# Kernel tuning notes

Hardware: AMD Instinct MI355X
Metric: run time of the kernel (lower is better)

The kernel has to match this reference:

```python
import jax, jax.numpy as jnp
import numpy as np

B, S, D, H = 4, 2048, 1024, 16
HS = D // H  # head size = 64


def setup_inputs() -> dict:
    key = jax.random.key(0)
    k1, k2, k3 = jax.random.split(key, 3)
    return {
        "input_data": jax.random.normal(k1, (B, S, D), dtype=jnp.float32),
        "w_qkv": jax.random.normal(k2, (D, 3 * D), dtype=jnp.float32) * (1.0 / np.sqrt(D)),
        "b_qkv": jnp.zeros((3 * D,), dtype=jnp.float32),
        "w_proj": jax.random.normal(k3, (D, D), dtype=jnp.float32) * (1.0 / np.sqrt(D)),
        "b_proj": jnp.zeros((D,), dtype=jnp.float32),
    }


def reference(input_data, w_qkv, b_qkv, w_proj, b_proj):
    b, s, d = input_data.shape
    qkv = input_data @ w_qkv + b_qkv  # [b, s, 3d]
    q, k, v = jnp.split(qkv, 3, axis=-1)
    # [b, h, s, hs]
    q = q.reshape(b, s, H, HS).transpose(0, 2, 1, 3)
    k = k.reshape(b, s, H, HS).transpose(0, 2, 1, 3)
    v = v.reshape(b, s, H, HS).transpose(0, 2, 1, 3)
    # NB: original module scales by 1/sqrt(num_heads), not 1/sqrt(head_size)
    scores = jnp.einsum('bhqd,bhkd->bhqk', q, k) / jnp.sqrt(jnp.float32(H))
    causal = jnp.tril(jnp.ones((s, s), dtype=bool))
    scores = jnp.where(causal[None, None], scores, -jnp.inf)
    weights = jax.nn.softmax(scores, axis=-1)  # dropout p=0.0 -> identity
    out = jnp.einsum('bhqk,bhkd->bhqd', weights, v)
    out = out.transpose(0, 2, 1, 3).reshape(b, s, d)
    return out @ w_proj + b_proj
```

## Files before the change

kernel.cpp:

```cpp
#include <hip/hip_runtime.h>


typedef unsigned short u16;
typedef short bf16x8 __attribute__((ext_vector_type(8)));
typedef unsigned short u16x8 __attribute__((ext_vector_type(8)));
typedef float f32x4 __attribute__((ext_vector_type(4)));
typedef float f32x16 __attribute__((ext_vector_type(16)));

#define S_LEN 2048
#define DMODEL 1024
#define NHEAD 16
#define MROWS 8192

#define SCALE_LOG2E 0.36067376022224085f

#define WAITVM_(N) asm volatile("s_waitcnt vmcnt(" #N ")" ::: "memory")
#define WAITVM(N) WAITVM_(N)

__device__ __forceinline__ u16 f2bf(float f) {
  union { float f; unsigned u; } c; c.f = f;
  unsigned u = c.u;
  u += 0x7fffu + ((u >> 16) & 1u);
  return (u16)(u >> 16);
}

__device__ __forceinline__ float exp2_fast(float x) {
  float r; asm("v_exp_f32 %0, %1" : "=v"(r) : "v"(x)); return r;
}

__device__ __forceinline__ unsigned cvtpk_bf16(float a, float b) {
  unsigned r;
  asm("v_cvt_pk_bf16_f32 %0, %1, %2" : "=v"(r) : "v"(a), "v"(b));
  return r;
}

__device__ __forceinline__ void plswap(unsigned& a, unsigned& b) {
  asm("v_permlane32_swap_b32 %0, %1" : "+v"(a), "+v"(b));
}

__device__ __forceinline__ f32x4 mfma16(bf16x8 a, bf16x8 b, f32x4 c) {
  return __builtin_amdgcn_mfma_f32_16x16x32_bf16(a, b, c, 0, 0, 0);
}

__device__ __forceinline__ f32x16 mfma32(bf16x8 a, bf16x8 b, f32x16 c) {
  return __builtin_amdgcn_mfma_f32_32x32x16_bf16(a, b, c, 0, 0, 0);
}

__device__ __forceinline__ void gload_lds16(const void* g, void* l) {
  __builtin_amdgcn_global_load_lds((__attribute__((address_space(1))) void*)g,
                                   (__attribute__((address_space(3))) void*)l,
                                   16, 0, 0);
}

__global__ void k_f32_to_bf16(const float* __restrict__ in, u16* __restrict__ out, int n) {
  int i = (blockIdx.x * 256 + threadIdx.x) * 4;
  if (i < n) {
    float4 v = *reinterpret_cast<const float4*>(in + i);
    ushort4 o;
    o.x = f2bf(v.x); o.y = f2bf(v.y); o.z = f2bf(v.z); o.w = f2bf(v.w);
    *reinterpret_cast<ushort4*>(out + i) = o;
  }
}

__global__ void k_transpose_to_bf16(const float* __restrict__ in, u16* __restrict__ out,
                                    int K, int N) {
  __shared__ float t[32][33];
  int n0 = blockIdx.x * 32, k0 = blockIdx.y * 32;
  int tx = threadIdx.x & 31, ty = threadIdx.x >> 5;
#pragma unroll
  for (int i = 0; i < 32; i += 8)
    t[ty + i][tx] = in[(size_t)(k0 + ty + i) * N + n0 + tx];
  __syncthreads();
#pragma unroll
  for (int i = 0; i < 32; i += 8)
    out[(size_t)(n0 + ty + i) * K + k0 + tx] = f2bf(t[tx][ty + i]);
}

template <int MODE, int BM>
__global__ __launch_bounds__(BM * 2) void k_gemm9(const u16* __restrict__ A,
                                                  const u16* __restrict__ Bt,
                                                  const float* __restrict__ bias,
                                                  u16* __restrict__ outb,
                                                  float* __restrict__ outf,
                                                  u16* __restrict__ vtout,
                                                  int N, int K) {
  constexpr int LOADS = (BM == 256) ? 3 : 4;
  __shared__ u16 As[3][BM * 32];
  __shared__ u16 Bs[3][128 * 32];

  const int tid = threadIdx.x;
  const int lane = tid & 63, wave = tid >> 6;
  const int wr = wave >> 1, wc = wave & 1;
  const int lr = lane & 15, lk = lane >> 4;
  const int m0 = blockIdx.x * BM, n0 = blockIdx.y * 128;
  const size_t Kb = (size_t)K * 2;

  const int csw = ((tid & 3) ^ ((tid >> 3) & 3)) * 16;
  const char* Asrc0 = (const char*)A + (size_t)(m0 + (tid >> 2)) * Kb + csw;
  const char* Asrc1 = Asrc0 + (size_t)(BM / 2) * Kb;
  const char* Bsrc0 = (const char*)Bt + (size_t)(n0 + (tid >> 2)) * Kb + csw;
  const char* Bsrc1 = Bsrc0 + (size_t)64 * Kb;

#define STAGE_T(BUFX, T)                                                       \
  {                                                                            \
    const size_t ko_ = (size_t)(T) * 64;                                       \
    gload_lds16(Asrc0 + ko_, &As[BUFX][(size_t)tid * 8]);                      \
    gload_lds16(Asrc1 + ko_, &As[BUFX][(size_t)tid * 8 + (size_t)BM * 16]);    \
    gload_lds16(Bsrc0 + ko_, &Bs[BUFX][(size_t)tid * 8]);                      \
    if (BM == 128)                                                             \
      gload_lds16(Bsrc1 + ko_, &Bs[BUFX][(size_t)tid * 8 + 2048]);             \
  }

  f32x4 zero4 = {0.f, 0.f, 0.f, 0.f};
  f32x4 acc[4][4];
#pragma unroll
  for (int m = 0; m < 4; ++m)
#pragma unroll
    for (int n = 0; n < 4; ++n) acc[m][n] = zero4;

  const int slotsw = (lr >> 1) & 3;

#define PHASE_T(BUFX, DOSTAGE, SBUF, ST, VMZERO)                               \
  {                                                                            \
    if (VMZERO) { WAITVM(0); }                                                 \
    else if (LOADS == 3) { WAITVM(3); }                                        \
    else { WAITVM(4); }                                                        \
    __builtin_amdgcn_s_barrier();                                              \
    __builtin_amdgcn_sched_barrier(0);                                         \
    bf16x8 af[4], bfr[4];                                                      \
    _Pragma("unroll") for (int m = 0; m < 4; ++m)                              \
        af[m] = *reinterpret_cast<const bf16x8*>(                              \
            &As[BUFX][(wr * 64 + m * 16 + lr) * 32 + ((lk ^ slotsw) * 8)]);    \
    _Pragma("unroll") for (int n = 0; n < 4; ++n)                              \
        bfr[n] = *reinterpret_cast<const bf16x8*>(                             \
            &Bs[BUFX][(wc * 64 + n * 16 + lr) * 32 + ((lk ^ slotsw) * 8)]);    \
    if (DOSTAGE) STAGE_T(SBUF, ST);                                            \
    __builtin_amdgcn_sched_barrier(0);                                         \
    __builtin_amdgcn_s_setprio(1);                                             \
    _Pragma("unroll") for (int m = 0; m < 4; ++m)                              \
        _Pragma("unroll") for (int n = 0; n < 4; ++n)                          \
            acc[m][n] = mfma16(af[m], bfr[n], acc[m][n]);                      \
    __builtin_amdgcn_s_setprio(0);                                             \
  }

  const int nkt = K >> 5;
  STAGE_T(0, 0);
  STAGE_T(1, 1);

  for (int t = 0; t < nkt - 2; ++t) {
    PHASE_T(t % 3, 1, (t + 2) % 3, t + 2, 0);
  }
  PHASE_T((nkt - 2) % 3, 0, 0, 0, 0);
  PHASE_T((nkt - 1) % 3, 0, 0, 0, 1);
#undef PHASE_T
#undef STAGE_T

#pragma unroll
  for (int n = 0; n < 4; ++n) {
    int col = n0 + wc * 64 + n * 16 + lr;
    float bv = bias[col];
#pragma unroll
    for (int m = 0; m < 4; ++m) {
      int rowb = m0 + wr * 64 + m * 16 + lk * 4;
      if (MODE == 1) {
#pragma unroll
        for (int r = 0; r < 4; ++r)
          outf[(size_t)(rowb + r) * N + col] = acc[m][n][r] + bv;
      } else {
        if (col < 2048) {
          const float qs = (col < 1024) ? SCALE_LOG2E : 1.0f;
#pragma unroll
          for (int r = 0; r < 4; ++r)
            outb[(size_t)(rowb + r) * 2048 + col] = f2bf((acc[m][n][r] + bv) * qs);
        } else {
          int hh = (col >> 6) & 15, dd = col & 63;
          int bb = rowb >> 11, ss = rowb & 2047;
          ushort4 o;
          o.x = f2bf(acc[m][n][0] + bv);
          o.y = f2bf(acc[m][n][1] + bv);
          o.z = f2bf(acc[m][n][2] + bv);
          o.w = f2bf(acc[m][n][3] + bv);
          *reinterpret_cast<ushort4*>(
              vtout + ((size_t)(bb * 16 + hh) * 64 + dd) * 2048 + ss) = o;
        }
      }
    }
  }
}

__global__ __launch_bounds__(256, 2) void k_attn14(const u16* __restrict__ qk,
                                                   const u16* __restrict__ vt,
                                                   u16* __restrict__ ao) {
  __shared__ u16 Ks[2][4096];
  __shared__ u16 Vs[2][4096];

  const int tid = threadIdx.x;
  const int lane = tid & 63, wave = tid >> 6;
  const int l31 = lane & 31, hi = lane >> 5;
  const int gid = blockIdx.x;
  const int bh = gid & 63;
  const int tq = gid >> 6;
  const int j = (tq < 4) ? tq : 11 - tq;
  const int b = bh >> 4, h = bh & 15;

  const int qbase = j * 256 + wave * 64;
  const int ktd = 4 * j + wave;
  const int KTMAX = 4 * j + 3;

  bf16x8 qf[2][4];
#pragma unroll
  for (int g = 0; g < 2; ++g) {
    const u16* qp = qk + ((size_t)b * S_LEN + qbase + g * 32 + l31) * 2048 + h * 64 + hi * 8;
#pragma unroll
    for (int ks = 0; ks < 4; ++ks)
      qf[g][ks] = *reinterpret_cast<const bf16x8*>(qp + ks * 16);
  }

  const int swzcol = 16 * ((lane & 7) ^ (lane >> 3));
  const char* kg = (const char*)qk + ((size_t)b * S_LEN) * 4096 + 2048 + h * 128 +
                   (size_t)(wave * 16 + (lane >> 3)) * 4096 + swzcol;
  const char* vg = (const char*)vt +
                   ((size_t)bh * 64 + wave * 16 + (lane >> 3)) * 4096 + swzcol;

#define STAGE(BUF, KT)                                                        \
  {                                                                           \
    const char* kg_ = kg + (size_t)(KT) * 64 * 4096;                          \
    const char* vg_ = vg + (size_t)(KT) * 128;                                \
    gload_lds16(kg_, &Ks[BUF][wave * 1024]);                                  \
    gload_lds16(kg_ + (size_t)8 * 4096, &Ks[BUF][wave * 1024 + 512]);         \
    gload_lds16(vg_, &Vs[BUF][wave * 1024]);                                  \
    gload_lds16(vg_ + (size_t)8 * 4096, &Vs[BUF][wave * 1024 + 512]);         \
  }

  f32x16 oT[2][2];
#pragma unroll
  for (int g = 0; g < 2; ++g)
#pragma unroll
    for (int kb = 0; kb < 2; ++kb)
#pragma unroll
      for (int e = 0; e < 16; ++e) oT[g][kb][e] = 0.f;
  float l_i[2] = {0.f, 0.f};

  const int rsw = (l31 & 7) << 4;

  STAGE(0, 0);
  __syncthreads();
  int buf = 0;

  for (int kt = 0; kt <= KTMAX; ++kt) {
    if (kt < KTMAX) STAGE(buf ^ 1, kt + 1);

    if (kt <= ktd) {
      const char* Kb = (const char*)&Ks[buf][0];
      const char* Vb = (const char*)&Vs[buf][0];
      const bool masked = (kt == ktd);

      bf16x8 kf[2][4];
#pragma unroll
      for (int kb = 0; kb < 2; ++kb)
#pragma unroll
        for (int ks = 0; ks < 4; ++ks)
          kf[kb][ks] = *reinterpret_cast<const bf16x8*>(
              Kb + (kb * 32 + l31) * 128 + ((ks * 32 + hi * 16) ^ rsw));

      bf16x8 vf[2][4];
#pragma unroll
      for (int kbd = 0; kbd < 2; ++kbd)
#pragma unroll
        for (int tt = 0; tt < 4; ++tt)
          vf[kbd][tt] = *reinterpret_cast<const bf16x8*>(
              Vb + (kbd * 32 + l31) * 128 + ((tt * 32 + hi * 16) ^ rsw));

#pragma unroll
      for (int g = 0; g < 2; ++g) {
        f32x16 sc[2];
        __builtin_amdgcn_s_setprio(1);
#pragma unroll
        for (int kb = 0; kb < 2; ++kb) {
          sc[kb] = mfma32(kf[kb][0], qf[g][0], f32x16{});
#pragma unroll
          for (int ks = 1; ks < 4; ++ks)
            sc[kb] = mfma32(kf[kb][ks], qf[g][ks], sc[kb]);
        }
        __builtin_amdgcn_s_setprio(0);

        if (masked) {
          const int qrel = g * 32 + l31;
#pragma unroll
          for (int kb = 0; kb < 2; ++kb)
#pragma unroll
            for (int e = 0; e < 16; ++e) {
              int key_ = kb * 32 + (e & 3) + ((e >> 2) << 3) + hi * 4;
              if (key_ > qrel) sc[kb][e] = -INFINITY;
            }
        }

        float rsa = 0.f, rsb = 0.f, rsc = 0.f, rsd = 0.f;
        unsigned pk_[8][2];
#pragma unroll
        for (int kb = 0; kb < 2; ++kb)
#pragma unroll
          for (int s = 0; s < 4; ++s) {
            float p0 = exp2_fast(sc[kb][s * 4 + 0]);
            float p1 = exp2_fast(sc[kb][s * 4 + 1]);
            float p2 = exp2_fast(sc[kb][s * 4 + 2]);
            float p3 = exp2_fast(sc[kb][s * 4 + 3]);
            rsa += p0; rsb += p1; rsc += p2; rsd += p3;
            pk_[kb * 4 + s][0] = cvtpk_bf16(p0, p1);
            pk_[kb * 4 + s][1] = cvtpk_bf16(p2, p3);
          }
        l_i[g] += (rsa + rsb) + (rsc + rsd);

        bf16x8 pfr[4];
#pragma unroll
        for (int tt = 0; tt < 4; ++tt) {
          unsigned a0 = pk_[2 * tt][0], b0 = pk_[2 * tt + 1][0];
          unsigned a1 = pk_[2 * tt][1], b1 = pk_[2 * tt + 1][1];
          plswap(a0, b0);
          plswap(a1, b1);
          unsigned fr[4] = {a0, a1, b0, b1};
          pfr[tt] = *reinterpret_cast<const bf16x8*>(&fr[0]);
        }

        __builtin_amdgcn_s_setprio(1);
#pragma unroll
        for (int tt = 0; tt < 4; ++tt) {
          oT[g][0] = mfma32(vf[0][tt], pfr[tt], oT[g][0]);
          oT[g][1] = mfma32(vf[1][tt], pfr[tt], oT[g][1]);
        }
        __builtin_amdgcn_s_setprio(0);
      }
    }

    __syncthreads();
    buf ^= 1;
  }
#undef STAGE

#pragma unroll
  for (int g = 0; g < 2; ++g) {
    float lt = l_i[g] + __shfl_xor(l_i[g], 32, 64);
    float inv = 1.f / lt;
    u16* orow = ao + ((size_t)b * S_LEN + qbase + g * 32 + l31) * DMODEL + h * 64 + hi * 4;
#pragma unroll
    for (int kbd = 0; kbd < 2; ++kbd)
#pragma unroll
      for (int s = 0; s < 4; ++s) {
        unsigned w0 = cvtpk_bf16(oT[g][kbd][s * 4 + 0] * inv, oT[g][kbd][s * 4 + 1] * inv);
        unsigned w1 = cvtpk_bf16(oT[g][kbd][s * 4 + 2] * inv, oT[g][kbd][s * 4 + 3] * inv);
        *reinterpret_cast<unsigned*>(orow + kbd * 32 + s * 8) = w0;
        *reinterpret_cast<unsigned*>(orow + kbd * 32 + s * 8 + 2) = w1;
      }
  }
}

extern "C" void kernel_launch(void* const* d_in, const int* in_sizes, int n_in,
                              void* d_out, int out_size, void* d_ws, size_t ws_size,
                              hipStream_t stream) {
  const float* x = (const float*)d_in[0];
  const float* wqkv = (const float*)d_in[1];
  const float* bqkv = (const float*)d_in[2];
  const float* wproj = (const float*)d_in[3];
  const float* bproj = (const float*)d_in[4];
  float* out = (float*)d_out;

  char* ws = (char*)d_ws;
  u16* Xb     = (u16*)(ws);
  u16* Wqkvt  = (u16*)(ws + (size_t)16777216);
  u16* Wprojt = (u16*)(ws + (size_t)23068672);
  u16* QKb    = (u16*)(ws + (size_t)25165824);
  u16* Vt     = (u16*)(ws + (size_t)58720256);
  u16* AOb    = (u16*)(ws + (size_t)75497472);

  k_f32_to_bf16<<<MROWS * DMODEL / 4 / 256, 256, 0, stream>>>(x, Xb, MROWS * DMODEL);
  k_transpose_to_bf16<<<dim3(3072 / 32, 1024 / 32), 256, 0, stream>>>(wqkv, Wqkvt, 1024, 3072);
  k_transpose_to_bf16<<<dim3(1024 / 32, 1024 / 32), 256, 0, stream>>>(wproj, Wprojt, 1024, 1024);

  k_gemm9<2, 256><<<dim3(MROWS / 256, 3072 / 128), 512, 0, stream>>>(
      Xb, Wqkvt, bqkv, QKb, nullptr, Vt, 3072, 1024);

  k_attn14<<<dim3(512), 256, 0, stream>>>(QKb, Vt, AOb);

  k_gemm9<1, 128><<<dim3(MROWS / 128, DMODEL / 128), 256, 0, stream>>>(
      AOb, Wprojt, bproj, nullptr, out, nullptr, DMODEL, 1024);
}
```

Measured before the change: 171.6 us.

## Double-buffer GEMM fragments in registers and deepen the LDS prefetch pipeline

Restructures the bf16 GEMM main loop so the LDS fragments for the next k-tile are read into a second register set while the MFMAs for the current tile run. Global-to-LDS staging now keeps three tiles in flight instead of two. N and K become compile-time constants so the loop fully unrolls with fixed waitcnt values. The aim is to hide LDS read latency behind the MFMA work and cut barrier stalls, at the cost of more vector registers for the extra fragment set and a waitcnt that is conservative for the 128-row variant.

```diff
diff --git a/kernel.cpp b/kernel.cpp
--- a/kernel.cpp
+++ b/kernel.cpp
@@ -16,6 +16,7 @@
 
 #define WAITVM_(N) asm volatile("s_waitcnt vmcnt(" #N ")" ::: "memory")
 #define WAITVM(N) WAITVM_(N)
+#define WAITLGKM0 asm volatile("s_waitcnt lgkmcnt(0)" ::: "memory")
 
 __device__ __forceinline__ u16 f2bf(float f) {
   union { float f; unsigned u; } c; c.f = f;
@@ -77,14 +78,14 @@
 }
 
 template <int MODE, int BM>
-__global__ __launch_bounds__(BM * 2) void k_gemm9(const u16* __restrict__ A,
-                                                  const u16* __restrict__ Bt,
-                                                  const float* __restrict__ bias,
-                                                  u16* __restrict__ outb,
-                                                  float* __restrict__ outf,
-                                                  u16* __restrict__ vtout,
-                                                  int N, int K) {
-  constexpr int LOADS = (BM == 256) ? 3 : 4;
+__global__ __launch_bounds__(BM * 2) void k_gemm10(const u16* __restrict__ A,
+                                                   const u16* __restrict__ Bt,
+                                                   const float* __restrict__ bias,
+                                                   u16* __restrict__ outb,
+                                                   float* __restrict__ outf,
+                                                   u16* __restrict__ vtout) {
+  const int N = (MODE == 2) ? 3072 : DMODEL;
+  const int K = 1024;
   __shared__ u16 As[3][BM * 32];
   __shared__ u16 Bs[3][128 * 32];
 
@@ -120,39 +121,59 @@
 
   const int slotsw = (lr >> 1) & 3;
 
-#define PHASE_T(BUFX, DOSTAGE, SBUF, ST, VMZERO)                               \
+#define READF(AF, BF, BUFX)                                                    \
   {                                                                            \
-    if (VMZERO) { WAITVM(0); }                                                 \
-    else if (LOADS == 3) { WAITVM(3); }                                        \
-    else { WAITVM(4); }                                                        \
-    __builtin_amdgcn_s_barrier();                                              \
-    __builtin_amdgcn_sched_barrier(0);                                         \
-    bf16x8 af[4], bfr[4];                                                      \
     _Pragma("unroll") for (int m = 0; m < 4; ++m)                              \
-        af[m] = *reinterpret_cast<const bf16x8*>(                              \
+        AF[m] = *reinterpret_cast<const bf16x8*>(                              \
             &As[BUFX][(wr * 64 + m * 16 + lr) * 32 + ((lk ^ slotsw) * 8)]);    \
     _Pragma("unroll") for (int n = 0; n < 4; ++n)                              \
-        bfr[n] = *reinterpret_cast<const bf16x8*>(                             \
+        BF[n] = *reinterpret_cast<const bf16x8*>(                              \
             &Bs[BUFX][(wc * 64 + n * 16 + lr) * 32 + ((lk ^ slotsw) * 8)]);    \
-    if (DOSTAGE) STAGE_T(SBUF, ST);                                            \
-    __builtin_amdgcn_sched_barrier(0);                                         \
+  }
+
+#define DOMFMA(AF, BF)                                                         \
+  {                                                                            \
     __builtin_amdgcn_s_setprio(1);                                             \
     _Pragma("unroll") for (int m = 0; m < 4; ++m)                              \
         _Pragma("unroll") for (int n = 0; n < 4; ++n)                          \
-            acc[m][n] = mfma16(af[m], bfr[n], acc[m][n]);                      \
+            acc[m][n] = mfma16(AF[m], BF[n], acc[m][n]);                       \
     __builtin_amdgcn_s_setprio(0);                                             \
   }
 
-  const int nkt = K >> 5;
+#define ITER(CA, CB, NA, NB, TT, DOSTAGE, VMN)                                 \
+  {                                                                            \
+    WAITLGKM0;                                                                 \
+    WAITVM(VMN);                                                               \
+    __builtin_amdgcn_sched_barrier(0);                                         \
+    __builtin_amdgcn_s_barrier();                                              \
+    __builtin_amdgcn_sched_barrier(0);                                         \
+    READF(NA, NB, ((TT) + 1) % 3);                                             \
+    if (DOSTAGE) STAGE_T((TT) % 3, (TT) + 3);                                  \
+    __builtin_amdgcn_sched_barrier(0);                                         \
+    DOMFMA(CA, CB);                                                            \
+  }
+
+  bf16x8 a0[4], b0[4], a1[4], b1[4];
+
   STAGE_T(0, 0);
   STAGE_T(1, 1);
-
-  for (int t = 0; t < nkt - 2; ++t) {
-    PHASE_T(t % 3, 1, (t + 2) % 3, t + 2, 0);
-  }
-  PHASE_T((nkt - 2) % 3, 0, 0, 0, 0);
-  PHASE_T((nkt - 1) % 3, 0, 0, 0, 1);
-#undef PHASE_T
+  STAGE_T(2, 2);
+  WAITVM(6);
+  __builtin_amdgcn_s_barrier();
+  READF(a0, b0, 0);
+
+  for (int t = 0; t < 28; t += 2) {
+    ITER(a0, b0, a1, b1, t, 1, 3);
+    ITER(a1, b1, a0, b0, t + 1, 1, 3);
+  }
+  ITER(a0, b0, a1, b1, 28, 1, 3);
+  ITER(a1, b1, a0, b0, 29, 0, 3);
+  ITER(a0, b0, a1, b1, 30, 0, 0);
+  WAITLGKM0;
+  DOMFMA(a1, b1);
+#undef ITER
+#undef DOMFMA
+#undef READF
 #undef STAGE_T
 
 #pragma unroll
@@ -376,11 +397,11 @@
   k_transpose_to_bf16<<<dim3(3072 / 32, 1024 / 32), 256, 0, stream>>>(wqkv, Wqkvt, 1024, 3072);
   k_transpose_to_bf16<<<dim3(1024 / 32, 1024 / 32), 256, 0, stream>>>(wproj, Wprojt, 1024, 1024);
 
-  k_gemm9<2, 256><<<dim3(MROWS / 256, 3072 / 128), 512, 0, stream>>>(
-      Xb, Wqkvt, bqkv, QKb, nullptr, Vt, 3072, 1024);
+  k_gemm10<2, 256><<<dim3(MROWS / 256, 3072 / 128), 512, 0, stream>>>(
+      Xb, Wqkvt, bqkv, QKb, nullptr, Vt);
 
   k_attn14<<<dim3(512), 256, 0, stream>>>(QKb, Vt, AOb);
 
-  k_gemm9<1, 128><<<dim3(MROWS / 128, DMODEL / 128), 256, 0, stream>>>(
-      AOb, Wprojt, bproj, nullptr, out, nullptr, DMODEL, 1024);
-}
+  k_gemm10<1, 128><<<dim3(MROWS / 128, DMODEL / 128), 256, 0, stream>>>(
+      AOb, Wprojt, bproj, nullptr, out, nullptr);
+}
```

Measured after the change: 169.9 us. No clear change (-1.0%).

## Retile GEMMs to 128x256 blocks with 4 waves each computing 128x64

Applied to the files above, without the earlier changes.

Replaces the templated GEMM (256x128 or 128x128 tiles, 2x2 wave grid) with a single 128x256 tile kernel where each of 4 waves covers all 128 rows and a 64-column slice. This doubles the per-wave accumulator tile to 8x4 MFMA blocks, raising MFMA work per LDS fragment load and per staged byte. It also hardcodes N and K as compile-time constants. The costs are higher register pressure (128 accumulator floats per lane), fewer blocks for the output projection (256 blocks), and more loads per stage with a deeper vmcnt wait.

```diff
diff --git a/kernel.cpp b/kernel.cpp
--- a/kernel.cpp
+++ b/kernel.cpp
@@ -76,45 +76,43 @@
     out[(size_t)(n0 + ty + i) * K + k0 + tx] = f2bf(t[tx][ty + i]);
 }
 
-template <int MODE, int BM>
-__global__ __launch_bounds__(BM * 2) void k_gemm9(const u16* __restrict__ A,
-                                                  const u16* __restrict__ Bt,
-                                                  const float* __restrict__ bias,
-                                                  u16* __restrict__ outb,
-                                                  float* __restrict__ outf,
-                                                  u16* __restrict__ vtout,
-                                                  int N, int K) {
-  constexpr int LOADS = (BM == 256) ? 3 : 4;
-  __shared__ u16 As[3][BM * 32];
-  __shared__ u16 Bs[3][128 * 32];
+template <int MODE>
+__global__ __launch_bounds__(256) void k_gemm11(const u16* __restrict__ A,
+                                                const u16* __restrict__ Bt,
+                                                const float* __restrict__ bias,
+                                                u16* __restrict__ outb,
+                                                float* __restrict__ outf,
+                                                u16* __restrict__ vtout) {
+  const int N = (MODE == 2) ? 3072 : DMODEL;
+  const int K = 1024;
+  __shared__ u16 As[3][128 * 32];
+  __shared__ u16 Bs[3][256 * 32];
 
   const int tid = threadIdx.x;
   const int lane = tid & 63, wave = tid >> 6;
-  const int wr = wave >> 1, wc = wave & 1;
   const int lr = lane & 15, lk = lane >> 4;
-  const int m0 = blockIdx.x * BM, n0 = blockIdx.y * 128;
+  const int m0 = blockIdx.x * 128, n0 = blockIdx.y * 256;
   const size_t Kb = (size_t)K * 2;
 
   const int csw = ((tid & 3) ^ ((tid >> 3) & 3)) * 16;
   const char* Asrc0 = (const char*)A + (size_t)(m0 + (tid >> 2)) * Kb + csw;
-  const char* Asrc1 = Asrc0 + (size_t)(BM / 2) * Kb;
   const char* Bsrc0 = (const char*)Bt + (size_t)(n0 + (tid >> 2)) * Kb + csw;
-  const char* Bsrc1 = Bsrc0 + (size_t)64 * Kb;
 
 #define STAGE_T(BUFX, T)                                                       \
   {                                                                            \
     const size_t ko_ = (size_t)(T) * 64;                                       \
     gload_lds16(Asrc0 + ko_, &As[BUFX][(size_t)tid * 8]);                      \
-    gload_lds16(Asrc1 + ko_, &As[BUFX][(size_t)tid * 8 + (size_t)BM * 16]);    \
+    gload_lds16(Asrc0 + (size_t)64 * Kb + ko_, &As[BUFX][(size_t)tid * 8 + 2048]); \
     gload_lds16(Bsrc0 + ko_, &Bs[BUFX][(size_t)tid * 8]);                      \
-    if (BM == 128)                                                             \
-      gload_lds16(Bsrc1 + ko_, &Bs[BUFX][(size_t)tid * 8 + 2048]);             \
+    gload_lds16(Bsrc0 + (size_t)64 * Kb + ko_, &Bs[BUFX][(size_t)tid * 8 + 2048]); \
+    gload_lds16(Bsrc0 + (size_t)128 * Kb + ko_, &Bs[BUFX][(size_t)tid * 8 + 4096]); \
+    gload_lds16(Bsrc0 + (size_t)192 * Kb + ko_, &Bs[BUFX][(size_t)tid * 8 + 6144]); \
   }
 
   f32x4 zero4 = {0.f, 0.f, 0.f, 0.f};
-  f32x4 acc[4][4];
-#pragma unroll
-  for (int m = 0; m < 4; ++m)
+  f32x4 acc[8][4];
+#pragma unroll
+  for (int m = 0; m < 8; ++m)
 #pragma unroll
     for (int n = 0; n < 4; ++n) acc[m][n] = zero4;
 
@@ -122,22 +120,20 @@
 
 #define PHASE_T(BUFX, DOSTAGE, SBUF, ST, VMZERO)                               \
   {                                                                            \
-    if (VMZERO) { WAITVM(0); }                                                 \
-    else if (LOADS == 3) { WAITVM(3); }                                        \
-    else { WAITVM(4); }                                                        \
+    if (VMZERO) { WAITVM(0); } else { WAITVM(6); }                             \
     __builtin_amdgcn_s_barrier();                                              \
     __builtin_amdgcn_sched_barrier(0);                                         \
-    bf16x8 af[4], bfr[4];                                                      \
-    _Pragma("unroll") for (int m = 0; m < 4; ++m)                              \
+    bf16x8 af[8], bfr[4];                                                      \
+    _Pragma("unroll") for (int m = 0; m < 8; ++m)                              \
         af[m] = *reinterpret_cast<const bf16x8*>(                              \
-            &As[BUFX][(wr * 64 + m * 16 + lr) * 32 + ((lk ^ slotsw) * 8)]);    \
+            &As[BUFX][(m * 16 + lr) * 32 + ((lk ^ slotsw) * 8)]);              \
     _Pragma("unroll") for (int n = 0; n < 4; ++n)                              \
         bfr[n] = *reinterpret_cast<const bf16x8*>(                             \
-            &Bs[BUFX][(wc * 64 + n * 16 + lr) * 32 + ((lk ^ slotsw) * 8)]);    \
+            &Bs[BUFX][(wave * 64 + n * 16 + lr) * 32 + ((lk ^ slotsw) * 8)]);  \
     if (DOSTAGE) STAGE_T(SBUF, ST);                                            \
     __builtin_amdgcn_sched_barrier(0);                                         \
     __builtin_amdgcn_s_setprio(1);                                             \
-    _Pragma("unroll") for (int m = 0; m < 4; ++m)                              \
+    _Pragma("unroll") for (int m = 0; m < 8; ++m)                              \
         _Pragma("unroll") for (int n = 0; n < 4; ++n)                          \
             acc[m][n] = mfma16(af[m], bfr[n], acc[m][n]);                      \
     __builtin_amdgcn_s_setprio(0);                                             \
@@ -157,11 +153,11 @@
 
 #pragma unroll
   for (int n = 0; n < 4; ++n) {
-    int col = n0 + wc * 64 + n * 16 + lr;
+    int col = n0 + wave * 64 + n * 16 + lr;
     float bv = bias[col];
 #pragma unroll
-    for (int m = 0; m < 4; ++m) {
-      int rowb = m0 + wr * 64 + m * 16 + lk * 4;
+    for (int m = 0; m < 8; ++m) {
+      int rowb = m0 + m * 16 + lk * 4;
       if (MODE == 1) {
 #pragma unroll
         for (int r = 0; r < 4; ++r)
@@ -376,11 +372,11 @@
   k_transpose_to_bf16<<<dim3(3072 / 32, 1024 / 32), 256, 0, stream>>>(wqkv, Wqkvt, 1024, 3072);
   k_transpose_to_bf16<<<dim3(1024 / 32, 1024 / 32), 256, 0, stream>>>(wproj, Wprojt, 1024, 1024);
 
-  k_gemm9<2, 256><<<dim3(MROWS / 256, 3072 / 128), 512, 0, stream>>>(
-      Xb, Wqkvt, bqkv, QKb, nullptr, Vt, 3072, 1024);
+  k_gemm11<2><<<dim3(MROWS / 128, 3072 / 256), 256, 0, stream>>>(
+      Xb, Wqkvt, bqkv, QKb, nullptr, Vt);
 
   k_attn14<<<dim3(512), 256, 0, stream>>>(QKb, Vt, AOb);
 
-  k_gemm9<1, 128><<<dim3(MROWS / 128, DMODEL / 128), 256, 0, stream>>>(
-      AOb, Wprojt, bproj, nullptr, out, nullptr, DMODEL, 1024);
-}
+  k_gemm11<1><<<dim3(MROWS / 128, DMODEL / 256), 256, 0, stream>>>(
+      AOb, Wprojt, bproj, nullptr, out, nullptr);
+}
```

New measurement: 190.2 us. 1.11x slower.
